# Kernel tuning notes

Hardware: AMD Instinct MI355X
Metric: run time of the kernel (lower is better)

## Reference

```python
import jax, jax.numpy as jnp
import numpy as np

EPS = 1e-5
SLOPE = 0.2

def _inorm(x):
    # InstanceNorm2d with affine=False on [B, C, N, 1]: normalize over spatial N per (b, c).
    mu = jnp.mean(x, axis=-1, keepdims=True)
    var = jnp.var(x, axis=-1, keepdims=True)  # biased variance, matches torch InstanceNorm
    return (x - mu) * jax.lax.rsqrt(var + EPS)

def _lrelu(x):
    return jnp.where(x >= 0, x, SLOPE * x)

def _block(W, x):
    # 1x1 conv (channel matmul) -> instance norm -> leaky relu; x: [B, Cin, N]
    return _lrelu(_inorm(jnp.einsum('oc,bcn->bon', W, x)))

def setup_inputs() -> dict:
    key = jax.random.key(0)
    k1, k2, k3, k4, k5 = jax.random.split(key, 5)
    B, C, N = 8, 256, 2048
    feat = jax.random.normal(k1, (B, C, N), dtype=jnp.float32)
    W1 = jax.random.normal(k2, (2 * C, C), dtype=jnp.float32) * (1.0 / np.sqrt(C))
    W2 = jax.random.normal(k3, (2 * C, C), dtype=jnp.float32) * (1.0 / np.sqrt(C))
    W3 = jax.random.normal(k4, (2 * C, C), dtype=jnp.float32) * (1.0 / np.sqrt(C))
    W4 = jax.random.normal(k5, (C, 2 * C), dtype=jnp.float32) * (1.0 / np.sqrt(2 * C))
    return {"feat": feat, "W1": W1, "W2": W2, "W3": W3, "W4": W4}

def reference(feat, W1, W2, W3, W4):
    # feat: [B, C, N]
    x1 = _block(W1, feat)  # [B, 2C, N]
    x2 = _block(W2, feat)  # [B, 2C, N]
    x3 = _block(W3, feat)  # [B, 2C, N]
    # query_key: x1^T @ x2 -> [B, N, N]
    qk = jnp.einsum('bcn,bcm->bnm', x1, x2)
    # x3 @ qk -> [B, 2C, N]; offset attention: subtract from x1
    x4 = x1 - jnp.einsum('bcn,bnm->bcm', x3, qk)
    out = _block(W4, x4)  # [B, C, N]
    return out
```

## Files before the change

kernel.cpp:

```cpp
#include <hip/hip_runtime.h>
#include <stdint.h>


#define LRELU_SLOPE 0.2f
#define EPS_IN 1e-5f

typedef __attribute__((ext_vector_type(8))) short short8v;
typedef __attribute__((ext_vector_type(4))) float f32x4;

__device__ __forceinline__ unsigned short f2bf(float f) {
    unsigned int u = __builtin_bit_cast(unsigned int, f);
    u = (u + 0x7fffu + ((u >> 16) & 1u)) >> 16;
    return (unsigned short)u;
}
__device__ __forceinline__ float bf2f(unsigned short h) {
    return __builtin_bit_cast(float, (unsigned int)h << 16);
}

typedef const __attribute__((address_space(1))) unsigned int* as1_uint_ptr;
typedef __attribute__((address_space(3))) unsigned int* as3_uint_ptr;

#define GLL16(g, l) __builtin_amdgcn_global_load_lds( \
    (as1_uint_ptr)(const void*)(g), (as3_uint_ptr)(void*)(l), 16, 0, 0)

enum { EP_F32 = 0, EP_BF16 = 1, EP_SUB_T_SPLIT = 2 };

template<int BM, int BN, int EP>
__global__ __launch_bounds__(256)
void gemm_tn(const unsigned short* __restrict__ A, const unsigned short* __restrict__ B,
             const unsigned short* __restrict__ Dm, void* __restrict__ Cv,
             int K, int lda, int ldb, int ldd, int ldc,
             int64_t sA, int64_t sB, int64_t sD, int64_t sC)
{
    constexpr int FM = BM / 32, FN = BN / 32;
    const int bz = blockIdx.z;
    A += sA * bz;
    B += sB * bz;

    const int i0 = blockIdx.y * BM;
    const int j0 = blockIdx.x * BN;

    __shared__ __align__(16) unsigned short As[BM * 32];
    __shared__ __align__(16) unsigned short Bs[BN * 32];

    const int t = threadIdx.x;
    const int w = t >> 6, l = t & 63;
    const int wr = w >> 1, wc = w & 1;

    f32x4 acc[FM][FN];
#pragma unroll
    for (int fm = 0; fm < FM; ++fm)
#pragma unroll
        for (int fn = 0; fn < FN; ++fn)
            acc[fm][fn] = (f32x4){0.f, 0.f, 0.f, 0.f};

    for (int k0 = 0; k0 < K; k0 += 32) {
        __syncthreads();
#pragma unroll
        for (int q = 0; q < BM / 64; ++q) {
            const int seg = w * (BM / 64) + q;
            const int row = seg * 16 + (l >> 2);
            const unsigned short* g = A + (size_t)(i0 + row) * lda + k0 + (l & 3) * 8;
            GLL16(g, &As[seg * 512]);
        }
#pragma unroll
        for (int q = 0; q < BN / 64; ++q) {
            const int seg = w * (BN / 64) + q;
            const int row = seg * 16 + (l >> 2);
            const unsigned short* g = B + (size_t)(j0 + row) * ldb + k0 + (l & 3) * 8;
            GLL16(g, &Bs[seg * 512]);
        }
        asm volatile("s_waitcnt vmcnt(0)" ::: "memory");
        __syncthreads();

        short8v a[FM], b[FN];
#pragma unroll
        for (int fm = 0; fm < FM; ++fm)
            a[fm] = *(const short8v*)&As[(wr * (BM / 2) + fm * 16 + (l & 15)) * 32 + (l >> 4) * 8];
#pragma unroll
        for (int fn = 0; fn < FN; ++fn)
            b[fn] = *(const short8v*)&Bs[(wc * (BN / 2) + fn * 16 + (l & 15)) * 32 + (l >> 4) * 8];
#pragma unroll
        for (int fm = 0; fm < FM; ++fm)
#pragma unroll
            for (int fn = 0; fn < FN; ++fn)
                acc[fm][fn] = __builtin_amdgcn_mfma_f32_16x16x32_bf16(a[fm], b[fn], acc[fm][fn], 0, 0, 0);
    }

    const int cr4 = (l >> 4) * 4;
    const int cc = l & 15;
#pragma unroll
    for (int fm = 0; fm < FM; ++fm) {
#pragma unroll
        for (int fn = 0; fn < FN; ++fn) {
            const int grow0 = i0 + wr * (BM / 2) + fm * 16 + cr4;
            const int gcol  = j0 + wc * (BN / 2) + fn * 16 + cc;
            if constexpr (EP == EP_F32) {
                float* C = (float*)Cv + sC * bz;
#pragma unroll
                for (int r = 0; r < 4; ++r)
                    C[(size_t)(grow0 + r) * ldc + gcol] = acc[fm][fn][r];
            } else if constexpr (EP == EP_BF16) {
                unsigned short* C = (unsigned short*)Cv + sC * bz;
#pragma unroll
                for (int r = 0; r < 4; ++r)
                    C[(size_t)(grow0 + r) * ldc + gcol] = f2bf(acc[fm][fn][r]);
            } else {
                const unsigned short* D = Dm + sD * bz;
                unsigned short* C = (unsigned short*)Cv + sC * bz;
                ushort4 hi4, lo4;
#pragma unroll
                for (int r = 0; r < 4; ++r) {
                    const float s = bf2f(D[(size_t)(grow0 + r) * ldd + gcol]) - acc[fm][fn][r];
                    const unsigned short h = f2bf(s);
                    const unsigned short lo = f2bf(s - bf2f(h));
                    ((unsigned short*)&hi4)[r] = h;
                    ((unsigned short*)&lo4)[r] = lo;
                }
                *(ushort4*)&C[(size_t)gcol * ldc + grow0] = hi4;
                *(ushort4*)&C[(size_t)gcol * ldc + (ldc >> 1) + grow0] = lo4;
            }
        }
    }
}

__global__ __launch_bounds__(256)
void row_norm_lrelu_bf16(unsigned short* __restrict__ y)
{
    const size_t row = blockIdx.x;
    uint4* p = (uint4*)(y + row * 2048);
    const int t = threadIdx.x;
    uint4 v = p[t];

    unsigned int wd[4] = {v.x, v.y, v.z, v.w};
    float f[8];
#pragma unroll
    for (int i = 0; i < 4; ++i) {
        f[2 * i]     = __builtin_bit_cast(float, wd[i] << 16);
        f[2 * i + 1] = __builtin_bit_cast(float, wd[i] & 0xffff0000u);
    }
    float s = 0.f, ss = 0.f;
#pragma unroll
    for (int i = 0; i < 8; ++i) { s += f[i]; ss += f[i] * f[i]; }

#pragma unroll
    for (int off = 32; off > 0; off >>= 1) {
        s  += __shfl_down(s, off, 64);
        ss += __shfl_down(ss, off, 64);
    }
    __shared__ float red[10];
    const int wid = t >> 6;
    if ((t & 63) == 0) { red[wid] = s; red[4 + wid] = ss; }
    __syncthreads();
    if (t == 0) {
        const float S  = red[0] + red[1] + red[2] + red[3];
        const float SS = red[4] + red[5] + red[6] + red[7];
        const float mu = S * (1.0f / 2048.0f);
        const float var = SS * (1.0f / 2048.0f) - mu * mu;
        red[8] = mu;
        red[9] = rsqrtf(var + EPS_IN);
    }
    __syncthreads();
    const float mu = red[8], rs = red[9];
#pragma unroll
    for (int i = 0; i < 8; ++i) {
        float e = (f[i] - mu) * rs;
        f[i] = (e >= 0.f) ? e : LRELU_SLOPE * e;
    }
#pragma unroll
    for (int i = 0; i < 4; ++i)
        wd[i] = (unsigned int)f2bf(f[2 * i]) | ((unsigned int)f2bf(f[2 * i + 1]) << 16);
    p[t] = make_uint4(wd[0], wd[1], wd[2], wd[3]);
}

__global__ __launch_bounds__(256)
void row_norm_lrelu(const float* __restrict__ in, float* __restrict__ out)
{
    const size_t row = blockIdx.x;
    const float4* p = (const float4*)(in + row * 2048);
    float4* q = (float4*)(out + row * 2048);
    const int t = threadIdx.x;

    float4 v0 = p[t];
    float4 v1 = p[t + 256];

    float s  = v0.x + v0.y + v0.z + v0.w + v1.x + v1.y + v1.z + v1.w;
    float ss = v0.x * v0.x + v0.y * v0.y + v0.z * v0.z + v0.w * v0.w +
               v1.x * v1.x + v1.y * v1.y + v1.z * v1.z + v1.w * v1.w;
#pragma unroll
    for (int off = 32; off > 0; off >>= 1) {
        s  += __shfl_down(s, off, 64);
        ss += __shfl_down(ss, off, 64);
    }
    __shared__ float red[10];
    const int wid = t >> 6;
    if ((t & 63) == 0) { red[wid] = s; red[4 + wid] = ss; }
    __syncthreads();
    if (t == 0) {
        const float S  = red[0] + red[1] + red[2] + red[3];
        const float SS = red[4] + red[5] + red[6] + red[7];
        const float mu = S * (1.0f / 2048.0f);
        const float var = SS * (1.0f / 2048.0f) - mu * mu;
        red[8] = mu;
        red[9] = rsqrtf(var + EPS_IN);
    }
    __syncthreads();
    const float mu = red[8], rs = red[9];
#define NRM(x) { float e = ((x) - mu) * rs; (x) = (e >= 0.0f) ? e : LRELU_SLOPE * e; }
    NRM(v0.x) NRM(v0.y) NRM(v0.z) NRM(v0.w)
    NRM(v1.x) NRM(v1.y) NRM(v1.z) NRM(v1.w)
#undef NRM
    q[t] = v0;
    q[t + 256] = v1;
}

template<bool F32IN>
__global__ __launch_bounds__(256)
void transpose_cast(const void* __restrict__ in, unsigned short* __restrict__ out,
                    int inCols, int outCols, int64_t sIn, int64_t sOut)
{
    __shared__ __align__(16) unsigned short tile[64][68];
    const int t = threadIdx.x;
    const int r0 = blockIdx.y * 64, c0 = blockIdx.x * 64;
    const int ir = t >> 4, ic = (t & 15) * 4;

#pragma unroll
    for (int q = 0; q < 4; ++q) {
        const int rr = q * 16 + ir;
        if constexpr (F32IN) {
            const float* ip = (const float*)in + sIn * blockIdx.z + (size_t)(r0 + rr) * inCols + c0 + ic;
            float4 v = *(const float4*)ip;
            tile[rr][ic + 0] = f2bf(v.x);
            tile[rr][ic + 1] = f2bf(v.y);
            tile[rr][ic + 2] = f2bf(v.z);
            tile[rr][ic + 3] = f2bf(v.w);
        } else {
            const unsigned short* ip = (const unsigned short*)in + sIn * blockIdx.z + (size_t)(r0 + rr) * inCols + c0 + ic;
            ushort4 v = *(const ushort4*)ip;
            tile[rr][ic + 0] = v.x;
            tile[rr][ic + 1] = v.y;
            tile[rr][ic + 2] = v.z;
            tile[rr][ic + 3] = v.w;
        }
    }
    __syncthreads();

    const int n = t & 63, kc = (t >> 6) * 16;
    unsigned short* op = out + sOut * blockIdx.z + (size_t)(c0 + n) * outCols + r0 + kc;
    unsigned int wo[8];
#pragma unroll
    for (int i = 0; i < 8; ++i)
        wo[i] = (unsigned int)tile[kc + 2 * i][n] | ((unsigned int)tile[kc + 2 * i + 1][n] << 16);
    *(uint4*)op       = make_uint4(wo[0], wo[1], wo[2], wo[3]);
    *(uint4*)(op + 8) = make_uint4(wo[4], wo[5], wo[6], wo[7]);
}

__global__ __launch_bounds__(256)
void cast_weights(const float* __restrict__ W1, const float* __restrict__ W2,
                  const float* __restrict__ W3, const float* __restrict__ W4,
                  unsigned short* __restrict__ Wcatb, unsigned short* __restrict__ W4cat)
{
    const int wsel = blockIdx.x >> 7;
    const int local = ((blockIdx.x & 127) * 256 + threadIdx.x) * 4;
    const float* src = (wsel == 0) ? W1 : (wsel == 1) ? W2 : (wsel == 2) ? W3 : W4;
    float4 v = *(const float4*)(src + local);
    ushort4 pk = make_ushort4(f2bf(v.x), f2bf(v.y), f2bf(v.z), f2bf(v.w));
    if (wsel < 3) {
        *(ushort4*)(Wcatb + (size_t)wsel * 131072 + local) = pk;
    } else {
        const int o = local >> 9, c = local & 511;
        *(ushort4*)(W4cat + (size_t)o * 1024 + c)       = pk;
        *(ushort4*)(W4cat + (size_t)o * 1024 + 512 + c) = pk;
    }
}

extern "C" void kernel_launch(void* const* d_in, const int* in_sizes, int n_in,
                              void* d_out, int out_size, void* d_ws, size_t ws_size,
                              hipStream_t stream)
{
    const float* feat = (const float*)d_in[0];
    const float* W1   = (const float*)d_in[1];
    const float* W2   = (const float*)d_in[2];
    const float* W3   = (const float*)d_in[3];
    const float* W4   = (const float*)d_in[4];
    float* out = (float*)d_out;

    char* w = (char*)d_ws;
    unsigned short* ybf   = (unsigned short*)(w + 0);
    unsigned short* featT = (unsigned short*)(w + 50331648);
    unsigned short* x2T   = (unsigned short*)(w + 58720256);
    unsigned short* Amb   = (unsigned short*)(w + 75497472);
    unsigned short* x4Ts  = (unsigned short*)(w + 79691776);
    float*          z     = (float*)(w + 113246208);
    unsigned short* Wcatb = (unsigned short*)(w + 130023424);
    unsigned short* W4cat = (unsigned short*)(w + 130809856);

    cast_weights<<<512, 256, 0, stream>>>(W1, W2, W3, W4, Wcatb, W4cat);

    transpose_cast<true><<<dim3(32, 4, 8), 256, 0, stream>>>(
        feat, featT, 2048, 256, 524288, 524288);

    gemm_tn<128, 128, EP_BF16><<<dim3(16, 12, 8), 256, 0, stream>>>(
        Wcatb, featT, nullptr, ybf,
        256, 256, 256, 0, 2048,
        0, 524288, 0, 3145728);

    row_norm_lrelu_bf16<<<12288, 256, 0, stream>>>(ybf);

    transpose_cast<false><<<dim3(32, 8, 8), 256, 0, stream>>>(
        ybf + 1048576, x2T, 2048, 512, 3145728, 1048576);

    gemm_tn<64, 64, EP_BF16><<<dim3(8, 8, 8), 256, 0, stream>>>(
        ybf + 2097152, ybf, nullptr, Amb,
        2048, 2048, 2048, 0, 512,
        3145728, 3145728, 0, 262144);

    gemm_tn<128, 128, EP_SUB_T_SPLIT><<<dim3(16, 4, 8), 256, 0, stream>>>(
        Amb, x2T, ybf, x4Ts,
        512, 512, 512, 2048, 1024,
        262144, 1048576, 3145728, 2097152);

    gemm_tn<128, 128, EP_F32><<<dim3(16, 2, 8), 256, 0, stream>>>(
        W4cat, x4Ts, nullptr, z,
        1024, 1024, 1024, 0, 2048,
        0, 2097152, 0, 524288);

    row_norm_lrelu<<<2048, 256, 0, stream>>>(z, out);
}
```

Measured before the change: 221.8 us.

## Fuse instance-norm statistics into GEMM epilogues and apply normalization on load

The first projection GEMM now emits per-row partial sums and sums of squares, and a small kernel reduces them to mean and rstd. The norm+lrelu is applied lazily where the data is consumed: when loading operands for the x3·x1 GEMM, in the x2 transpose, and in the subtract epilogue. This removes the separate read-modify-write normalization pass over the large activation buffer. The final GEMM becomes a cooperative kernel that computes row stats, does a grid-wide sync and writes the normalized output directly, dropping the fp32 intermediate and its norm kernel. In exchange the attention GEMM loses its async global-to-LDS loads in favour of register loads plus normalization, and the cooperative launch needs all 256 blocks resident at once.

```diff
diff --git a/kernel.cpp b/kernel.cpp
--- a/kernel.cpp
+++ b/kernel.cpp
@@ -1,4 +1,5 @@
 #include <hip/hip_runtime.h>
+#include <hip/hip_cooperative_groups.h>
 #include <stdint.h>
 
 
@@ -23,12 +24,13 @@
 #define GLL16(g, l) __builtin_amdgcn_global_load_lds( \
     (as1_uint_ptr)(const void*)(g), (as3_uint_ptr)(void*)(l), 16, 0, 0)
 
-enum { EP_F32 = 0, EP_BF16 = 1, EP_SUB_T_SPLIT = 2 };
+enum { EP_BF16_STATS = 0, EP_SUB_T_SPLIT_NORM = 1 };
 
 template<int BM, int BN, int EP>
 __global__ __launch_bounds__(256)
 void gemm_tn(const unsigned short* __restrict__ A, const unsigned short* __restrict__ B,
              const unsigned short* __restrict__ Dm, void* __restrict__ Cv,
+             const float2* __restrict__ stats, float2* __restrict__ part,
              int K, int lda, int ldb, int ldd, int ldc,
              int64_t sA, int64_t sB, int64_t sD, int64_t sC)
 {
@@ -60,15 +62,13 @@
         for (int q = 0; q < BM / 64; ++q) {
             const int seg = w * (BM / 64) + q;
             const int row = seg * 16 + (l >> 2);
-            const unsigned short* g = A + (size_t)(i0 + row) * lda + k0 + (l & 3) * 8;
-            GLL16(g, &As[seg * 512]);
+            GLL16(A + (size_t)(i0 + row) * lda + k0 + (l & 3) * 8, &As[seg * 512]);
         }
 #pragma unroll
         for (int q = 0; q < BN / 64; ++q) {
             const int seg = w * (BN / 64) + q;
             const int row = seg * 16 + (l >> 2);
-            const unsigned short* g = B + (size_t)(j0 + row) * ldb + k0 + (l & 3) * 8;
-            GLL16(g, &Bs[seg * 512]);
+            GLL16(B + (size_t)(j0 + row) * ldb + k0 + (l & 3) * 8, &Bs[seg * 512]);
         }
         asm volatile("s_waitcnt vmcnt(0)" ::: "memory");
         __syncthreads();
@@ -89,33 +89,58 @@
 
     const int cr4 = (l >> 4) * 4;
     const int cc = l & 15;
-#pragma unroll
-    for (int fm = 0; fm < FM; ++fm) {
-#pragma unroll
-        for (int fn = 0; fn < FN; ++fn) {
+
+    if constexpr (EP == EP_BF16_STATS) {
+        unsigned short* C = (unsigned short*)Cv + sC * bz;
+        __shared__ float2 wp[2][BM];
+#pragma unroll
+        for (int fm = 0; fm < FM; ++fm) {
+#pragma unroll
+            for (int r = 0; r < 4; ++r) {
+                float s = 0.f, q = 0.f;
+#pragma unroll
+                for (int fn = 0; fn < FN; ++fn) {
+                    const float v = acc[fm][fn][r];
+                    s += v; q += v * v;
+                    C[(size_t)(i0 + wr * (BM / 2) + fm * 16 + cr4 + r) * ldc +
+                      (j0 + wc * (BN / 2) + fn * 16 + cc)] = f2bf(v);
+                }
+#pragma unroll
+                for (int m = 1; m < 16; m <<= 1) {
+                    s += __shfl_xor(s, m, 64);
+                    q += __shfl_xor(q, m, 64);
+                }
+                if ((l & 15) == 0)
+                    wp[wc][wr * (BM / 2) + fm * 16 + cr4 + r] = make_float2(s, q);
+            }
+        }
+        __syncthreads();
+        if (t < BM) {
+            const float2 p0 = wp[0][t], p1 = wp[1][t];
+            part[(size_t)(bz * 1536 + i0 + t) * gridDim.x + blockIdx.x] =
+                make_float2(p0.x + p1.x, p0.y + p1.y);
+        }
+    } else {
+        const unsigned short* D = Dm + sD * bz;
+        unsigned short* C = (unsigned short*)Cv + sC * bz;
+#pragma unroll
+        for (int fm = 0; fm < FM; ++fm) {
             const int grow0 = i0 + wr * (BM / 2) + fm * 16 + cr4;
-            const int gcol  = j0 + wc * (BN / 2) + fn * 16 + cc;
-            if constexpr (EP == EP_F32) {
-                float* C = (float*)Cv + sC * bz;
-#pragma unroll
-                for (int r = 0; r < 4; ++r)
-                    C[(size_t)(grow0 + r) * ldc + gcol] = acc[fm][fn][r];
-            } else if constexpr (EP == EP_BF16) {
-                unsigned short* C = (unsigned short*)Cv + sC * bz;
-#pragma unroll
-                for (int r = 0; r < 4; ++r)
-                    C[(size_t)(grow0 + r) * ldc + gcol] = f2bf(acc[fm][fn][r]);
-            } else {
-                const unsigned short* D = Dm + sD * bz;
-                unsigned short* C = (unsigned short*)Cv + sC * bz;
+            float2 st[4];
+#pragma unroll
+            for (int r = 0; r < 4; ++r) st[r] = stats[bz * 1536 + grow0 + r];
+#pragma unroll
+            for (int fn = 0; fn < FN; ++fn) {
+                const int gcol = j0 + wc * (BN / 2) + fn * 16 + cc;
                 ushort4 hi4, lo4;
 #pragma unroll
                 for (int r = 0; r < 4; ++r) {
-                    const float s = bf2f(D[(size_t)(grow0 + r) * ldd + gcol]) - acc[fm][fn][r];
-                    const unsigned short h = f2bf(s);
-                    const unsigned short lo = f2bf(s - bf2f(h));
+                    float dv = (bf2f(D[(size_t)(grow0 + r) * ldd + gcol]) - st[r].x) * st[r].y;
+                    dv = dv >= 0.f ? dv : LRELU_SLOPE * dv;
+                    const float sv = dv - acc[fm][fn][r];
+                    const unsigned short h = f2bf(sv);
                     ((unsigned short*)&hi4)[r] = h;
-                    ((unsigned short*)&lo4)[r] = lo;
+                    ((unsigned short*)&lo4)[r] = f2bf(sv - bf2f(h));
                 }
                 *(ushort4*)&C[(size_t)gcol * ldc + grow0] = hi4;
                 *(ushort4*)&C[(size_t)gcol * ldc + (ldc >> 1) + grow0] = lo4;
@@ -125,128 +150,244 @@
 }
 
 __global__ __launch_bounds__(256)
-void row_norm_lrelu_bf16(unsigned short* __restrict__ y)
-{
-    const size_t row = blockIdx.x;
-    uint4* p = (uint4*)(y + row * 2048);
-    const int t = threadIdx.x;
-    uint4 v = p[t];
-
-    unsigned int wd[4] = {v.x, v.y, v.z, v.w};
-    float f[8];
+void reduce_stats(const float2* __restrict__ part, float2* __restrict__ stats)
+{
+    const int row = blockIdx.x * 256 + threadIdx.x;
+    float S = 0.f, Q = 0.f;
+#pragma unroll
+    for (int j = 0; j < 16; ++j) {
+        const float2 p = part[(size_t)row * 16 + j];
+        S += p.x; Q += p.y;
+    }
+    const float mu = S * (1.0f / 2048.0f);
+    const float var = Q * (1.0f / 2048.0f) - mu * mu;
+    stats[row] = make_float2(mu, rsqrtf(var + EPS_IN));
+}
+
+__device__ __forceinline__ void norm_store8(unsigned short* dst, uint4 v, float2 st)
+{
+    const unsigned int wd[4] = {v.x, v.y, v.z, v.w};
+    unsigned int o[4];
 #pragma unroll
     for (int i = 0; i < 4; ++i) {
-        f[2 * i]     = __builtin_bit_cast(float, wd[i] << 16);
-        f[2 * i + 1] = __builtin_bit_cast(float, wd[i] & 0xffff0000u);
-    }
-    float s = 0.f, ss = 0.f;
-#pragma unroll
-    for (int i = 0; i < 8; ++i) { s += f[i]; ss += f[i] * f[i]; }
-
-#pragma unroll
-    for (int off = 32; off > 0; off >>= 1) {
-        s  += __shfl_down(s, off, 64);
-        ss += __shfl_down(ss, off, 64);
-    }
-    __shared__ float red[10];
-    const int wid = t >> 6;
-    if ((t & 63) == 0) { red[wid] = s; red[4 + wid] = ss; }
+        float a = __builtin_bit_cast(float, wd[i] << 16);
+        float b = __builtin_bit_cast(float, wd[i] & 0xffff0000u);
+        a = (a - st.x) * st.y; a = a >= 0.f ? a : LRELU_SLOPE * a;
+        b = (b - st.x) * st.y; b = b >= 0.f ? b : LRELU_SLOPE * b;
+        o[i] = (unsigned int)f2bf(a) | ((unsigned int)f2bf(b) << 16);
+    }
+    *(uint4*)dst = make_uint4(o[0], o[1], o[2], o[3]);
+}
+
+__global__ __launch_bounds__(256)
+void gemm_am(const unsigned short* __restrict__ ybf, const float2* __restrict__ stats,
+             unsigned short* __restrict__ Amb)
+{
+    const int bz = blockIdx.z;
+    const unsigned short* Yb = ybf + (size_t)bz * 3145728;
+    const int i0 = blockIdx.y * 128;
+    const int j0 = blockIdx.x * 64;
+
+    __shared__ __align__(16) unsigned short As[128 * 32];
+    __shared__ __align__(16) unsigned short Bs[64 * 32];
+
+    const int t = threadIdx.x, w = t >> 6, l = t & 63;
+    const int wr = w >> 1, wc = w & 1;
+    const int lr = l >> 2, lk = (l & 3) * 8;
+
+    const int rA0 = i0 + (w * 2 + 0) * 16 + lr;
+    const int rA1 = i0 + (w * 2 + 1) * 16 + lr;
+    const int rB  = j0 + w * 16 + lr;
+    const float2 stA0 = stats[bz * 1536 + 1024 + rA0];
+    const float2 stA1 = stats[bz * 1536 + 1024 + rA1];
+    const float2 stB  = stats[bz * 1536 + rB];
+    const unsigned short* gA0 = Yb + (size_t)(1024 + rA0) * 2048 + lk;
+    const unsigned short* gA1 = Yb + (size_t)(1024 + rA1) * 2048 + lk;
+    const unsigned short* gB  = Yb + (size_t)rB * 2048 + lk;
+
+    f32x4 acc[4][2];
+#pragma unroll
+    for (int fm = 0; fm < 4; ++fm)
+#pragma unroll
+        for (int fn = 0; fn < 2; ++fn)
+            acc[fm][fn] = (f32x4){0.f, 0.f, 0.f, 0.f};
+
+    for (int k0 = 0; k0 < 2048; k0 += 32) {
+        const uint4 vA0 = *(const uint4*)(gA0 + k0);
+        const uint4 vA1 = *(const uint4*)(gA1 + k0);
+        const uint4 vB  = *(const uint4*)(gB + k0);
+        __syncthreads();
+        norm_store8(&As[(w * 2 + 0) * 512 + l * 8], vA0, stA0);
+        norm_store8(&As[(w * 2 + 1) * 512 + l * 8], vA1, stA1);
+        norm_store8(&Bs[w * 512 + l * 8], vB, stB);
+        __syncthreads();
+
+        short8v a[4], b[2];
+#pragma unroll
+        for (int fm = 0; fm < 4; ++fm)
+            a[fm] = *(const short8v*)&As[(wr * 64 + fm * 16 + (l & 15)) * 32 + (l >> 4) * 8];
+#pragma unroll
+        for (int fn = 0; fn < 2; ++fn)
+            b[fn] = *(const short8v*)&Bs[(wc * 32 + fn * 16 + (l & 15)) * 32 + (l >> 4) * 8];
+#pragma unroll
+        for (int fm = 0; fm < 4; ++fm)
+#pragma unroll
+            for (int fn = 0; fn < 2; ++fn)
+                acc[fm][fn] = __builtin_amdgcn_mfma_f32_16x16x32_bf16(a[fm], b[fn], acc[fm][fn], 0, 0, 0);
+    }
+
+    unsigned short* C = Amb + (size_t)bz * 262144;
+    const int cr4 = (l >> 4) * 4, cc = l & 15;
+#pragma unroll
+    for (int fm = 0; fm < 4; ++fm)
+#pragma unroll
+        for (int fn = 0; fn < 2; ++fn)
+#pragma unroll
+            for (int r = 0; r < 4; ++r)
+                C[(size_t)(i0 + wr * 64 + fm * 16 + cr4 + r) * 512 +
+                  (j0 + wc * 32 + fn * 16 + cc)] = f2bf(acc[fm][fn][r]);
+}
+
+__global__ __launch_bounds__(256)
+void gemm_z_coop(const unsigned short* __restrict__ A, const unsigned short* __restrict__ Bg,
+                 float2* __restrict__ zpart, float* __restrict__ out)
+{
+    const int bz = blockIdx.z;
+    const unsigned short* B = Bg + (size_t)bz * 2097152;
+    const int i0 = blockIdx.y * 128;
+    const int j0 = blockIdx.x * 128;
+
+    __shared__ __align__(16) unsigned short As[128 * 32];
+    __shared__ __align__(16) unsigned short Bs[128 * 32];
+
+    const int t = threadIdx.x, w = t >> 6, l = t & 63;
+    const int wr = w >> 1, wc = w & 1;
+
+    f32x4 acc[4][4];
+#pragma unroll
+    for (int fm = 0; fm < 4; ++fm)
+#pragma unroll
+        for (int fn = 0; fn < 4; ++fn)
+            acc[fm][fn] = (f32x4){0.f, 0.f, 0.f, 0.f};
+
+    for (int k0 = 0; k0 < 1024; k0 += 32) {
+        __syncthreads();
+#pragma unroll
+        for (int q = 0; q < 2; ++q) {
+            const int seg = w * 2 + q;
+            const int row = seg * 16 + (l >> 2);
+            GLL16(A + (size_t)(i0 + row) * 1024 + k0 + (l & 3) * 8, &As[seg * 512]);
+            GLL16(B + (size_t)(j0 + row) * 1024 + k0 + (l & 3) * 8, &Bs[seg * 512]);
+        }
+        asm volatile("s_waitcnt vmcnt(0)" ::: "memory");
+        __syncthreads();
+
+        short8v a[4], b[4];
+#pragma unroll
+        for (int fm = 0; fm < 4; ++fm)
+            a[fm] = *(const short8v*)&As[(wr * 64 + fm * 16 + (l & 15)) * 32 + (l >> 4) * 8];
+#pragma unroll
+        for (int fn = 0; fn < 4; ++fn)
+            b[fn] = *(const short8v*)&Bs[(wc * 64 + fn * 16 + (l & 15)) * 32 + (l >> 4) * 8];
+#pragma unroll
+        for (int fm = 0; fm < 4; ++fm)
+#pragma unroll
+            for (int fn = 0; fn < 4; ++fn)
+                acc[fm][fn] = __builtin_amdgcn_mfma_f32_16x16x32_bf16(a[fm], b[fn], acc[fm][fn], 0, 0, 0);
+    }
+
+    const int cr4 = (l >> 4) * 4, cc = l & 15;
+
+    __shared__ float2 wp[2][128];
+#pragma unroll
+    for (int fm = 0; fm < 4; ++fm) {
+#pragma unroll
+        for (int r = 0; r < 4; ++r) {
+            float s = 0.f, q = 0.f;
+#pragma unroll
+            for (int fn = 0; fn < 4; ++fn) {
+                const float v = acc[fm][fn][r];
+                s += v; q += v * v;
+            }
+#pragma unroll
+            for (int m = 1; m < 16; m <<= 1) {
+                s += __shfl_xor(s, m, 64);
+                q += __shfl_xor(q, m, 64);
+            }
+            if ((l & 15) == 0) wp[wc][wr * 64 + fm * 16 + cr4 + r] = make_float2(s, q);
+        }
+    }
     __syncthreads();
-    if (t == 0) {
-        const float S  = red[0] + red[1] + red[2] + red[3];
-        const float SS = red[4] + red[5] + red[6] + red[7];
+    if (t < 128) {
+        const float2 p0 = wp[0][t], p1 = wp[1][t];
+        zpart[((size_t)bz * 256 + i0 + t) * 16 + blockIdx.x] = make_float2(p0.x + p1.x, p0.y + p1.y);
+    }
+    __threadfence();
+    cooperative_groups::this_grid().sync();
+
+    __shared__ float2 rst[128];
+    if (t < 128) {
+        float S = 0.f, Q = 0.f;
+#pragma unroll
+        for (int j = 0; j < 16; ++j) {
+            const float2 p = zpart[((size_t)bz * 256 + i0 + t) * 16 + j];
+            S += p.x; Q += p.y;
+        }
         const float mu = S * (1.0f / 2048.0f);
-        const float var = SS * (1.0f / 2048.0f) - mu * mu;
-        red[8] = mu;
-        red[9] = rsqrtf(var + EPS_IN);
+        const float var = Q * (1.0f / 2048.0f) - mu * mu;
+        rst[t] = make_float2(mu, rsqrtf(var + EPS_IN));
     }
     __syncthreads();
-    const float mu = red[8], rs = red[9];
-#pragma unroll
-    for (int i = 0; i < 8; ++i) {
-        float e = (f[i] - mu) * rs;
-        f[i] = (e >= 0.f) ? e : LRELU_SLOPE * e;
-    }
-#pragma unroll
-    for (int i = 0; i < 4; ++i)
-        wd[i] = (unsigned int)f2bf(f[2 * i]) | ((unsigned int)f2bf(f[2 * i + 1]) << 16);
-    p[t] = make_uint4(wd[0], wd[1], wd[2], wd[3]);
-}
-
-__global__ __launch_bounds__(256)
-void row_norm_lrelu(const float* __restrict__ in, float* __restrict__ out)
-{
-    const size_t row = blockIdx.x;
-    const float4* p = (const float4*)(in + row * 2048);
-    float4* q = (float4*)(out + row * 2048);
-    const int t = threadIdx.x;
-
-    float4 v0 = p[t];
-    float4 v1 = p[t + 256];
-
-    float s  = v0.x + v0.y + v0.z + v0.w + v1.x + v1.y + v1.z + v1.w;
-    float ss = v0.x * v0.x + v0.y * v0.y + v0.z * v0.z + v0.w * v0.w +
-               v1.x * v1.x + v1.y * v1.y + v1.z * v1.z + v1.w * v1.w;
-#pragma unroll
-    for (int off = 32; off > 0; off >>= 1) {
-        s  += __shfl_down(s, off, 64);
-        ss += __shfl_down(ss, off, 64);
-    }
-    __shared__ float red[10];
-    const int wid = t >> 6;
-    if ((t & 63) == 0) { red[wid] = s; red[4 + wid] = ss; }
-    __syncthreads();
-    if (t == 0) {
-        const float S  = red[0] + red[1] + red[2] + red[3];
-        const float SS = red[4] + red[5] + red[6] + red[7];
-        const float mu = S * (1.0f / 2048.0f);
-        const float var = SS * (1.0f / 2048.0f) - mu * mu;
-        red[8] = mu;
-        red[9] = rsqrtf(var + EPS_IN);
-    }
-    __syncthreads();
-    const float mu = red[8], rs = red[9];
-#define NRM(x) { float e = ((x) - mu) * rs; (x) = (e >= 0.0f) ? e : LRELU_SLOPE * e; }
-    NRM(v0.x) NRM(v0.y) NRM(v0.z) NRM(v0.w)
-    NRM(v1.x) NRM(v1.y) NRM(v1.z) NRM(v1.w)
-#undef NRM
-    q[t] = v0;
-    q[t + 256] = v1;
-}
-
-template<bool F32IN>
-__global__ __launch_bounds__(256)
-void transpose_cast(const void* __restrict__ in, unsigned short* __restrict__ out,
-                    int inCols, int outCols, int64_t sIn, int64_t sOut)
+
+    float* O = out + (size_t)bz * 524288;
+#pragma unroll
+    for (int fm = 0; fm < 4; ++fm) {
+        const int lrow0 = wr * 64 + fm * 16 + cr4;
+        float2 st[4];
+#pragma unroll
+        for (int r = 0; r < 4; ++r) st[r] = rst[lrow0 + r];
+#pragma unroll
+        for (int fn = 0; fn < 4; ++fn) {
+            const int gcol = j0 + wc * 64 + fn * 16 + cc;
+#pragma unroll
+            for (int r = 0; r < 4; ++r) {
+                float e = (acc[fm][fn][r] - st[r].x) * st[r].y;
+                e = e >= 0.f ? e : LRELU_SLOPE * e;
+                O[(size_t)(i0 + lrow0 + r) * 2048 + gcol] = e;
+            }
+        }
+    }
+}
+
+__global__ __launch_bounds__(256)
+void transpose_norm_x2(const unsigned short* __restrict__ ybf,
+                       const float2* __restrict__ stats,
+                       unsigned short* __restrict__ x2T)
 {
     __shared__ __align__(16) unsigned short tile[64][68];
-    const int t = threadIdx.x;
+    const int t = threadIdx.x, bz = blockIdx.z;
+    const unsigned short* in = ybf + (size_t)bz * 3145728 + (size_t)512 * 2048;
+    unsigned short* outp = x2T + (size_t)bz * 1048576;
     const int r0 = blockIdx.y * 64, c0 = blockIdx.x * 64;
     const int ir = t >> 4, ic = (t & 15) * 4;
 
 #pragma unroll
     for (int q = 0; q < 4; ++q) {
         const int rr = q * 16 + ir;
-        if constexpr (F32IN) {
-            const float* ip = (const float*)in + sIn * blockIdx.z + (size_t)(r0 + rr) * inCols + c0 + ic;
-            float4 v = *(const float4*)ip;
-            tile[rr][ic + 0] = f2bf(v.x);
-            tile[rr][ic + 1] = f2bf(v.y);
-            tile[rr][ic + 2] = f2bf(v.z);
-            tile[rr][ic + 3] = f2bf(v.w);
-        } else {
-            const unsigned short* ip = (const unsigned short*)in + sIn * blockIdx.z + (size_t)(r0 + rr) * inCols + c0 + ic;
-            ushort4 v = *(const ushort4*)ip;
-            tile[rr][ic + 0] = v.x;
-            tile[rr][ic + 1] = v.y;
-            tile[rr][ic + 2] = v.z;
-            tile[rr][ic + 3] = v.w;
+        const float2 st = stats[bz * 1536 + 512 + r0 + rr];
+        const ushort4 v = *(const ushort4*)&in[(size_t)(r0 + rr) * 2048 + c0 + ic];
+        const unsigned short vv[4] = {v.x, v.y, v.z, v.w};
+#pragma unroll
+        for (int j = 0; j < 4; ++j) {
+            float e = (bf2f(vv[j]) - st.x) * st.y;
+            e = e >= 0.f ? e : LRELU_SLOPE * e;
+            tile[rr][ic + j] = f2bf(e);
         }
     }
     __syncthreads();
 
     const int n = t & 63, kc = (t >> 6) * 16;
-    unsigned short* op = out + sOut * blockIdx.z + (size_t)(c0 + n) * outCols + r0 + kc;
+    unsigned short* op = outp + (size_t)(c0 + n) * 512 + r0 + kc;
     unsigned int wo[8];
 #pragma unroll
     for (int i = 0; i < 8; ++i)
@@ -256,6 +397,37 @@
 }
 
 __global__ __launch_bounds__(256)
+void transpose_feat(const float* __restrict__ in, unsigned short* __restrict__ out)
+{
+    __shared__ __align__(16) unsigned short tile[64][68];
+    const int t = threadIdx.x, bz = blockIdx.z;
+    const float* ip0 = in + (size_t)bz * 524288;
+    unsigned short* outp = out + (size_t)bz * 524288;
+    const int r0 = blockIdx.y * 64, c0 = blockIdx.x * 64;
+    const int ir = t >> 4, ic = (t & 15) * 4;
+
+#pragma unroll
+    for (int q = 0; q < 4; ++q) {
+        const int rr = q * 16 + ir;
+        const float4 v = *(const float4*)&ip0[(size_t)(r0 + rr) * 2048 + c0 + ic];
+        tile[rr][ic + 0] = f2bf(v.x);
+        tile[rr][ic + 1] = f2bf(v.y);
+        tile[rr][ic + 2] = f2bf(v.z);
+        tile[rr][ic + 3] = f2bf(v.w);
+    }
+    __syncthreads();
+
+    const int n = t & 63, kc = (t >> 6) * 16;
+    unsigned short* op = outp + (size_t)(c0 + n) * 256 + r0 + kc;
+    unsigned int wo[8];
+#pragma unroll
+    for (int i = 0; i < 8; ++i)
+        wo[i] = (unsigned int)tile[kc + 2 * i][n] | ((unsigned int)tile[kc + 2 * i + 1][n] << 16);
+    *(uint4*)op       = make_uint4(wo[0], wo[1], wo[2], wo[3]);
+    *(uint4*)(op + 8) = make_uint4(wo[4], wo[5], wo[6], wo[7]);
+}
+
+__global__ __launch_bounds__(256)
 void cast_weights(const float* __restrict__ W1, const float* __restrict__ W2,
                   const float* __restrict__ W3, const float* __restrict__ W4,
                   unsigned short* __restrict__ Wcatb, unsigned short* __restrict__ W4cat)
@@ -263,8 +435,8 @@
     const int wsel = blockIdx.x >> 7;
     const int local = ((blockIdx.x & 127) * 256 + threadIdx.x) * 4;
     const float* src = (wsel == 0) ? W1 : (wsel == 1) ? W2 : (wsel == 2) ? W3 : W4;
-    float4 v = *(const float4*)(src + local);
-    ushort4 pk = make_ushort4(f2bf(v.x), f2bf(v.y), f2bf(v.z), f2bf(v.w));
+    const float4 v = *(const float4*)(src + local);
+    const ushort4 pk = make_ushort4(f2bf(v.x), f2bf(v.y), f2bf(v.z), f2bf(v.w));
     if (wsel < 3) {
         *(ushort4*)(Wcatb + (size_t)wsel * 131072 + local) = pk;
     } else {
@@ -291,39 +463,37 @@
     unsigned short* x2T   = (unsigned short*)(w + 58720256);
     unsigned short* Amb   = (unsigned short*)(w + 75497472);
     unsigned short* x4Ts  = (unsigned short*)(w + 79691776);
-    float*          z     = (float*)(w + 113246208);
-    unsigned short* Wcatb = (unsigned short*)(w + 130023424);
-    unsigned short* W4cat = (unsigned short*)(w + 130809856);
+    unsigned short* Wcatb = (unsigned short*)(w + 113246208);
+    unsigned short* W4cat = (unsigned short*)(w + 114032640);
+    float2*         part1 = (float2*)(w + 114556928);
+    float2*         stats = (float2*)(w + 116129792);
+    float2*         zpart = (float2*)(w + 116228096);
 
     cast_weights<<<512, 256, 0, stream>>>(W1, W2, W3, W4, Wcatb, W4cat);
 
-    transpose_cast<true><<<dim3(32, 4, 8), 256, 0, stream>>>(
-        feat, featT, 2048, 256, 524288, 524288);
-
-    gemm_tn<128, 128, EP_BF16><<<dim3(16, 12, 8), 256, 0, stream>>>(
-        Wcatb, featT, nullptr, ybf,
-        256, 256, 256, 0, 2048,
-        0, 524288, 0, 3145728);
-
-    row_norm_lrelu_bf16<<<12288, 256, 0, stream>>>(ybf);
-
-    transpose_cast<false><<<dim3(32, 8, 8), 256, 0, stream>>>(
-        ybf + 1048576, x2T, 2048, 512, 3145728, 1048576);
-
-    gemm_tn<64, 64, EP_BF16><<<dim3(8, 8, 8), 256, 0, stream>>>(
-        ybf + 2097152, ybf, nullptr, Amb,
-        2048, 2048, 2048, 0, 512,
-        3145728, 3145728, 0, 262144);
-
-    gemm_tn<128, 128, EP_SUB_T_SPLIT><<<dim3(16, 4, 8), 256, 0, stream>>>(
-        Amb, x2T, ybf, x4Ts,
-        512, 512, 512, 2048, 1024,
-        262144, 1048576, 3145728, 2097152);
-
-    gemm_tn<128, 128, EP_F32><<<dim3(16, 2, 8), 256, 0, stream>>>(
-        W4cat, x4Ts, nullptr, z,
-        1024, 1024, 1024, 0, 2048,
-        0, 2097152, 0, 524288);
-
-    row_norm_lrelu<<<2048, 256, 0, stream>>>(z, out);
-}
+    transpose_feat<<<dim3(32, 4, 8), 256, 0, stream>>>(feat, featT);
+
+    gemm_tn<128, 128, EP_BF16_STATS><<<dim3(16, 12, 8), 256, 0, stream>>>(
+        Wcatb, featT, nullptr, ybf, nullptr, part1,
+        256, 256, 256, 0, 2048, 0, 524288, 0, 3145728);
+
+    reduce_stats<<<48, 256, 0, stream>>>(part1, stats);
+
+    transpose_norm_x2<<<dim3(32, 8, 8), 256, 0, stream>>>(ybf, stats, x2T);
+
+    gemm_am<<<dim3(8, 4, 8), 256, 0, stream>>>(ybf, stats, Amb);
+
+    gemm_tn<128, 128, EP_SUB_T_SPLIT_NORM><<<dim3(16, 4, 8), 256, 0, stream>>>(
+        Amb, x2T, ybf, x4Ts, stats, nullptr,
+        512, 512, 512, 2048, 1024, 262144, 1048576, 3145728, 2097152);
+
+    {
+        const unsigned short* a0 = W4cat;
+        const unsigned short* b0 = x4Ts;
+        float2* zp = zpart;
+        float* o0 = out;
+        void* zargs[4] = {&a0, &b0, &zp, &o0};
+        hipLaunchCooperativeKernel((const void*)gemm_z_coop, dim3(16, 2, 8),
+                                   dim3(256, 1, 1), zargs, 0, stream);
+    }
+}
```

After: 346.3 us. +56.1%, slower.

## Fuse instance-norm statistics into first GEMM epilogue and normalize during transpose

Applied to the files above, without the earlier changes.

The first projection GEMM now computes per-row partial sums and sums of squares in its epilogue, and a small kernel reduces them into mean and rstd. This replaces the separate in-place row-norm pass over the 12288 rows. Normalization and leaky ReLU are applied while transposing x2 and while copying x1/x3 into a compact buffer, so the statistics are no longer recomputed from bf16 reads. The last GEMM's tile changes to 128x64 for more blocks, and the workspace layout is repacked. The cost is an extra reduction launch, a norm copy kernel, and statistics taken from fp32 accumulators rather than bf16-rounded values.

```diff
diff --git a/kernel.cpp b/kernel.cpp
--- a/kernel.cpp
+++ b/kernel.cpp
@@ -23,12 +23,13 @@
 #define GLL16(g, l) __builtin_amdgcn_global_load_lds( \
     (as1_uint_ptr)(const void*)(g), (as3_uint_ptr)(void*)(l), 16, 0, 0)
 
-enum { EP_F32 = 0, EP_BF16 = 1, EP_SUB_T_SPLIT = 2 };
+enum { EP_F32 = 0, EP_BF16 = 1, EP_SUB_T_SPLIT = 2, EP_BF16_STATS = 3 };
 
 template<int BM, int BN, int EP>
 __global__ __launch_bounds__(256)
 void gemm_tn(const unsigned short* __restrict__ A, const unsigned short* __restrict__ B,
              const unsigned short* __restrict__ Dm, void* __restrict__ Cv,
+             float2* __restrict__ part,
              int K, int lda, int ldb, int ldd, int ldc,
              int64_t sA, int64_t sB, int64_t sD, int64_t sC)
 {
@@ -60,15 +61,13 @@
         for (int q = 0; q < BM / 64; ++q) {
             const int seg = w * (BM / 64) + q;
             const int row = seg * 16 + (l >> 2);
-            const unsigned short* g = A + (size_t)(i0 + row) * lda + k0 + (l & 3) * 8;
-            GLL16(g, &As[seg * 512]);
+            GLL16(A + (size_t)(i0 + row) * lda + k0 + (l & 3) * 8, &As[seg * 512]);
         }
 #pragma unroll
         for (int q = 0; q < BN / 64; ++q) {
             const int seg = w * (BN / 64) + q;
             const int row = seg * 16 + (l >> 2);
-            const unsigned short* g = B + (size_t)(j0 + row) * ldb + k0 + (l & 3) * 8;
-            GLL16(g, &Bs[seg * 512]);
+            GLL16(B + (size_t)(j0 + row) * ldb + k0 + (l & 3) * 8, &Bs[seg * 512]);
         }
         asm volatile("s_waitcnt vmcnt(0)" ::: "memory");
         __syncthreads();
@@ -89,60 +88,205 @@
 
     const int cr4 = (l >> 4) * 4;
     const int cc = l & 15;
-#pragma unroll
-    for (int fm = 0; fm < FM; ++fm) {
-#pragma unroll
-        for (int fn = 0; fn < FN; ++fn) {
+
+    if constexpr (EP == EP_F32) {
+        float* C = (float*)Cv + sC * bz;
+#pragma unroll
+        for (int fm = 0; fm < FM; ++fm)
+#pragma unroll
+            for (int fn = 0; fn < FN; ++fn)
+#pragma unroll
+                for (int r = 0; r < 4; ++r)
+                    C[(size_t)(i0 + wr * (BM / 2) + fm * 16 + cr4 + r) * ldc +
+                      (j0 + wc * (BN / 2) + fn * 16 + cc)] = acc[fm][fn][r];
+    } else if constexpr (EP == EP_BF16) {
+        unsigned short* C = (unsigned short*)Cv + sC * bz;
+#pragma unroll
+        for (int fm = 0; fm < FM; ++fm)
+#pragma unroll
+            for (int fn = 0; fn < FN; ++fn)
+#pragma unroll
+                for (int r = 0; r < 4; ++r)
+                    C[(size_t)(i0 + wr * (BM / 2) + fm * 16 + cr4 + r) * ldc +
+                      (j0 + wc * (BN / 2) + fn * 16 + cc)] = f2bf(acc[fm][fn][r]);
+    } else if constexpr (EP == EP_SUB_T_SPLIT) {
+        const unsigned short* D = Dm + sD * bz;
+        unsigned short* C = (unsigned short*)Cv + sC * bz;
+#pragma unroll
+        for (int fm = 0; fm < FM; ++fm) {
             const int grow0 = i0 + wr * (BM / 2) + fm * 16 + cr4;
-            const int gcol  = j0 + wc * (BN / 2) + fn * 16 + cc;
-            if constexpr (EP == EP_F32) {
-                float* C = (float*)Cv + sC * bz;
-#pragma unroll
-                for (int r = 0; r < 4; ++r)
-                    C[(size_t)(grow0 + r) * ldc + gcol] = acc[fm][fn][r];
-            } else if constexpr (EP == EP_BF16) {
-                unsigned short* C = (unsigned short*)Cv + sC * bz;
-#pragma unroll
-                for (int r = 0; r < 4; ++r)
-                    C[(size_t)(grow0 + r) * ldc + gcol] = f2bf(acc[fm][fn][r]);
-            } else {
-                const unsigned short* D = Dm + sD * bz;
-                unsigned short* C = (unsigned short*)Cv + sC * bz;
+#pragma unroll
+            for (int fn = 0; fn < FN; ++fn) {
+                const int gcol = j0 + wc * (BN / 2) + fn * 16 + cc;
                 ushort4 hi4, lo4;
 #pragma unroll
                 for (int r = 0; r < 4; ++r) {
-                    const float s = bf2f(D[(size_t)(grow0 + r) * ldd + gcol]) - acc[fm][fn][r];
-                    const unsigned short h = f2bf(s);
-                    const unsigned short lo = f2bf(s - bf2f(h));
+                    const float sv = bf2f(D[(size_t)(grow0 + r) * ldd + gcol]) - acc[fm][fn][r];
+                    const unsigned short h = f2bf(sv);
                     ((unsigned short*)&hi4)[r] = h;
-                    ((unsigned short*)&lo4)[r] = lo;
+                    ((unsigned short*)&lo4)[r] = f2bf(sv - bf2f(h));
                 }
                 *(ushort4*)&C[(size_t)gcol * ldc + grow0] = hi4;
                 *(ushort4*)&C[(size_t)gcol * ldc + (ldc >> 1) + grow0] = lo4;
             }
         }
-    }
-}
-
-__global__ __launch_bounds__(256)
-void row_norm_lrelu_bf16(unsigned short* __restrict__ y)
+    } else {
+        unsigned short* C = (unsigned short*)Cv + sC * bz;
+        __shared__ float2 wp[2][BM];
+#pragma unroll
+        for (int fm = 0; fm < FM; ++fm) {
+#pragma unroll
+            for (int r = 0; r < 4; ++r) {
+                float s = 0.f, q = 0.f;
+#pragma unroll
+                for (int fn = 0; fn < FN; ++fn) {
+                    const float v = acc[fm][fn][r];
+                    s += v; q += v * v;
+                    C[(size_t)(i0 + wr * (BM / 2) + fm * 16 + cr4 + r) * ldc +
+                      (j0 + wc * (BN / 2) + fn * 16 + cc)] = f2bf(v);
+                }
+#pragma unroll
+                for (int m = 1; m < 16; m <<= 1) {
+                    s += __shfl_xor(s, m, 64);
+                    q += __shfl_xor(q, m, 64);
+                }
+                if ((l & 15) == 0)
+                    wp[wc][wr * (BM / 2) + fm * 16 + cr4 + r] = make_float2(s, q);
+            }
+        }
+        __syncthreads();
+        if (t < BM) {
+            const float2 p0 = wp[0][t], p1 = wp[1][t];
+            part[(size_t)(bz * 1536 + i0 + t) * gridDim.x + blockIdx.x] =
+                make_float2(p0.x + p1.x, p0.y + p1.y);
+        }
+    }
+}
+
+__global__ __launch_bounds__(256)
+void reduce_stats(const float2* __restrict__ part, float2* __restrict__ stats)
+{
+    const int row = blockIdx.x * 256 + threadIdx.x;
+    float S = 0.f, Q = 0.f;
+#pragma unroll
+    for (int j = 0; j < 16; ++j) {
+        const float2 p = part[(size_t)row * 16 + j];
+        S += p.x; Q += p.y;
+    }
+    const float mu = S * (1.0f / 2048.0f);
+    const float var = Q * (1.0f / 2048.0f) - mu * mu;
+    stats[row] = make_float2(mu, rsqrtf(var + EPS_IN));
+}
+
+__device__ __forceinline__ uint4 norm8(uint4 v, float2 st)
+{
+    const unsigned int wd[4] = {v.x, v.y, v.z, v.w};
+    unsigned int o[4];
+#pragma unroll
+    for (int i = 0; i < 4; ++i) {
+        float a = __builtin_bit_cast(float, wd[i] << 16);
+        float b = __builtin_bit_cast(float, wd[i] & 0xffff0000u);
+        a = (a - st.x) * st.y; a = a >= 0.f ? a : LRELU_SLOPE * a;
+        b = (b - st.x) * st.y; b = b >= 0.f ? b : LRELU_SLOPE * b;
+        o[i] = (unsigned int)f2bf(a) | ((unsigned int)f2bf(b) << 16);
+    }
+    return make_uint4(o[0], o[1], o[2], o[3]);
+}
+
+__global__ __launch_bounds__(256)
+void norm12(const unsigned short* __restrict__ ybf, const float2* __restrict__ stats,
+            unsigned short* __restrict__ x1n3)
+{
+    const int bz = blockIdx.y;
+    const int x = blockIdx.x;
+    const int src = (x < 512) ? x : (x + 512);
+    const float2 st = stats[bz * 1536 + src];
+    const uint4 v = ((const uint4*)(ybf + (size_t)bz * 3145728 + (size_t)src * 2048))[threadIdx.x];
+    ((uint4*)(x1n3 + (size_t)bz * 2097152 + (size_t)x * 2048))[threadIdx.x] = norm8(v, st);
+}
+
+__global__ __launch_bounds__(256)
+void transpose_norm_x2(const unsigned short* __restrict__ ybf,
+                       const float2* __restrict__ stats,
+                       unsigned short* __restrict__ x2T)
+{
+    __shared__ __align__(16) unsigned short tile[64][68];
+    const int t = threadIdx.x, bz = blockIdx.z;
+    const unsigned short* in = ybf + (size_t)bz * 3145728 + (size_t)512 * 2048;
+    unsigned short* outp = x2T + (size_t)bz * 1048576;
+    const int r0 = blockIdx.y * 64, c0 = blockIdx.x * 64;
+    const int ir = t >> 4, ic = (t & 15) * 4;
+
+#pragma unroll
+    for (int q = 0; q < 4; ++q) {
+        const int rr = q * 16 + ir;
+        const float2 st = stats[bz * 1536 + 512 + r0 + rr];
+        const ushort4 v = *(const ushort4*)&in[(size_t)(r0 + rr) * 2048 + c0 + ic];
+        const unsigned short vv[4] = {v.x, v.y, v.z, v.w};
+#pragma unroll
+        for (int j = 0; j < 4; ++j) {
+            float e = (bf2f(vv[j]) - st.x) * st.y;
+            e = e >= 0.f ? e : LRELU_SLOPE * e;
+            tile[rr][ic + j] = f2bf(e);
+        }
+    }
+    __syncthreads();
+
+    const int n = t & 63, kc = (t >> 6) * 16;
+    unsigned short* op = outp + (size_t)(c0 + n) * 512 + r0 + kc;
+    unsigned int wo[8];
+#pragma unroll
+    for (int i = 0; i < 8; ++i)
+        wo[i] = (unsigned int)tile[kc + 2 * i][n] | ((unsigned int)tile[kc + 2 * i + 1][n] << 16);
+    *(uint4*)op       = make_uint4(wo[0], wo[1], wo[2], wo[3]);
+    *(uint4*)(op + 8) = make_uint4(wo[4], wo[5], wo[6], wo[7]);
+}
+
+__global__ __launch_bounds__(256)
+void transpose_feat(const float* __restrict__ in, unsigned short* __restrict__ out)
+{
+    __shared__ __align__(16) unsigned short tile[64][68];
+    const int t = threadIdx.x, bz = blockIdx.z;
+    const float* ip0 = in + (size_t)bz * 524288;
+    unsigned short* outp = out + (size_t)bz * 524288;
+    const int r0 = blockIdx.y * 64, c0 = blockIdx.x * 64;
+    const int ir = t >> 4, ic = (t & 15) * 4;
+
+#pragma unroll
+    for (int q = 0; q < 4; ++q) {
+        const int rr = q * 16 + ir;
+        const float4 v = *(const float4*)&ip0[(size_t)(r0 + rr) * 2048 + c0 + ic];
+        tile[rr][ic + 0] = f2bf(v.x);
+        tile[rr][ic + 1] = f2bf(v.y);
+        tile[rr][ic + 2] = f2bf(v.z);
+        tile[rr][ic + 3] = f2bf(v.w);
+    }
+    __syncthreads();
+
+    const int n = t & 63, kc = (t >> 6) * 16;
+    unsigned short* op = outp + (size_t)(c0 + n) * 256 + r0 + kc;
+    unsigned int wo[8];
+#pragma unroll
+    for (int i = 0; i < 8; ++i)
+        wo[i] = (unsigned int)tile[kc + 2 * i][n] | ((unsigned int)tile[kc + 2 * i + 1][n] << 16);
+    *(uint4*)op       = make_uint4(wo[0], wo[1], wo[2], wo[3]);
+    *(uint4*)(op + 8) = make_uint4(wo[4], wo[5], wo[6], wo[7]);
+}
+
+__global__ __launch_bounds__(256)
+void row_norm_lrelu(const float* __restrict__ in, float* __restrict__ out)
 {
     const size_t row = blockIdx.x;
-    uint4* p = (uint4*)(y + row * 2048);
+    const float4* p = (const float4*)(in + row * 2048);
+    float4* q = (float4*)(out + row * 2048);
     const int t = threadIdx.x;
-    uint4 v = p[t];
-
-    unsigned int wd[4] = {v.x, v.y, v.z, v.w};
-    float f[8];
-#pragma unroll
-    for (int i = 0; i < 4; ++i) {
-        f[2 * i]     = __builtin_bit_cast(float, wd[i] << 16);
-        f[2 * i + 1] = __builtin_bit_cast(float, wd[i] & 0xffff0000u);
-    }
-    float s = 0.f, ss = 0.f;
-#pragma unroll
-    for (int i = 0; i < 8; ++i) { s += f[i]; ss += f[i] * f[i]; }
-
+
+    float4 v0 = p[t];
+    float4 v1 = p[t + 256];
+
+    float s  = v0.x + v0.y + v0.z + v0.w + v1.x + v1.y + v1.z + v1.w;
+    float ss = v0.x * v0.x + v0.y * v0.y + v0.z * v0.z + v0.w * v0.w +
+               v1.x * v1.x + v1.y * v1.y + v1.z * v1.z + v1.w * v1.w;
 #pragma unroll
     for (int off = 32; off > 0; off >>= 1) {
         s  += __shfl_down(s, off, 64);
@@ -162,50 +306,6 @@
     }
     __syncthreads();
     const float mu = red[8], rs = red[9];
-#pragma unroll
-    for (int i = 0; i < 8; ++i) {
-        float e = (f[i] - mu) * rs;
-        f[i] = (e >= 0.f) ? e : LRELU_SLOPE * e;
-    }
-#pragma unroll
-    for (int i = 0; i < 4; ++i)
-        wd[i] = (unsigned int)f2bf(f[2 * i]) | ((unsigned int)f2bf(f[2 * i + 1]) << 16);
-    p[t] = make_uint4(wd[0], wd[1], wd[2], wd[3]);
-}
-
-__global__ __launch_bounds__(256)
-void row_norm_lrelu(const float* __restrict__ in, float* __restrict__ out)
-{
-    const size_t row = blockIdx.x;
-    const float4* p = (const float4*)(in + row * 2048);
-    float4* q = (float4*)(out + row * 2048);
-    const int t = threadIdx.x;
-
-    float4 v0 = p[t];
-    float4 v1 = p[t + 256];
-
-    float s  = v0.x + v0.y + v0.z + v0.w + v1.x + v1.y + v1.z + v1.w;
-    float ss = v0.x * v0.x + v0.y * v0.y + v0.z * v0.z + v0.w * v0.w +
-               v1.x * v1.x + v1.y * v1.y + v1.z * v1.z + v1.w * v1.w;
-#pragma unroll
-    for (int off = 32; off > 0; off >>= 1) {
-        s  += __shfl_down(s, off, 64);
-        ss += __shfl_down(ss, off, 64);
-    }
-    __shared__ float red[10];
-    const int wid = t >> 6;
-    if ((t & 63) == 0) { red[wid] = s; red[4 + wid] = ss; }
-    __syncthreads();
-    if (t == 0) {
-        const float S  = red[0] + red[1] + red[2] + red[3];
-        const float SS = red[4] + red[5] + red[6] + red[7];
-        const float mu = S * (1.0f / 2048.0f);
-        const float var = SS * (1.0f / 2048.0f) - mu * mu;
-        red[8] = mu;
-        red[9] = rsqrtf(var + EPS_IN);
-    }
-    __syncthreads();
-    const float mu = red[8], rs = red[9];
 #define NRM(x) { float e = ((x) - mu) * rs; (x) = (e >= 0.0f) ? e : LRELU_SLOPE * e; }
     NRM(v0.x) NRM(v0.y) NRM(v0.z) NRM(v0.w)
     NRM(v1.x) NRM(v1.y) NRM(v1.z) NRM(v1.w)
@@ -214,47 +314,6 @@
     q[t + 256] = v1;
 }
 
-template<bool F32IN>
-__global__ __launch_bounds__(256)
-void transpose_cast(const void* __restrict__ in, unsigned short* __restrict__ out,
-                    int inCols, int outCols, int64_t sIn, int64_t sOut)
-{
-    __shared__ __align__(16) unsigned short tile[64][68];
-    const int t = threadIdx.x;
-    const int r0 = blockIdx.y * 64, c0 = blockIdx.x * 64;
-    const int ir = t >> 4, ic = (t & 15) * 4;
-
-#pragma unroll
-    for (int q = 0; q < 4; ++q) {
-        const int rr = q * 16 + ir;
-        if constexpr (F32IN) {
-            const float* ip = (const float*)in + sIn * blockIdx.z + (size_t)(r0 + rr) * inCols + c0 + ic;
-            float4 v = *(const float4*)ip;
-            tile[rr][ic + 0] = f2bf(v.x);
-            tile[rr][ic + 1] = f2bf(v.y);
-            tile[rr][ic + 2] = f2bf(v.z);
-            tile[rr][ic + 3] = f2bf(v.w);
-        } else {
-            const unsigned short* ip = (const unsigned short*)in + sIn * blockIdx.z + (size_t)(r0 + rr) * inCols + c0 + ic;
-            ushort4 v = *(const ushort4*)ip;
-            tile[rr][ic + 0] = v.x;
-            tile[rr][ic + 1] = v.y;
-            tile[rr][ic + 2] = v.z;
-            tile[rr][ic + 3] = v.w;
-        }
-    }
-    __syncthreads();
-
-    const int n = t & 63, kc = (t >> 6) * 16;
-    unsigned short* op = out + sOut * blockIdx.z + (size_t)(c0 + n) * outCols + r0 + kc;
-    unsigned int wo[8];
-#pragma unroll
-    for (int i = 0; i < 8; ++i)
-        wo[i] = (unsigned int)tile[kc + 2 * i][n] | ((unsigned int)tile[kc + 2 * i + 1][n] << 16);
-    *(uint4*)op       = make_uint4(wo[0], wo[1], wo[2], wo[3]);
-    *(uint4*)(op + 8) = make_uint4(wo[4], wo[5], wo[6], wo[7]);
-}
-
 __global__ __launch_bounds__(256)
 void cast_weights(const float* __restrict__ W1, const float* __restrict__ W2,
                   const float* __restrict__ W3, const float* __restrict__ W4,
@@ -263,8 +322,8 @@
     const int wsel = blockIdx.x >> 7;
     const int local = ((blockIdx.x & 127) * 256 + threadIdx.x) * 4;
     const float* src = (wsel == 0) ? W1 : (wsel == 1) ? W2 : (wsel == 2) ? W3 : W4;
-    float4 v = *(const float4*)(src + local);
-    ushort4 pk = make_ushort4(f2bf(v.x), f2bf(v.y), f2bf(v.z), f2bf(v.w));
+    const float4 v = *(const float4*)(src + local);
+    const ushort4 pk = make_ushort4(f2bf(v.x), f2bf(v.y), f2bf(v.z), f2bf(v.w));
     if (wsel < 3) {
         *(ushort4*)(Wcatb + (size_t)wsel * 131072 + local) = pk;
     } else {
@@ -287,43 +346,41 @@
 
     char* w = (char*)d_ws;
     unsigned short* ybf   = (unsigned short*)(w + 0);
+    unsigned short* x4Ts  = (unsigned short*)(w + 0);
+    float*          z     = (float*)(w + 33554432);
     unsigned short* featT = (unsigned short*)(w + 50331648);
     unsigned short* x2T   = (unsigned short*)(w + 58720256);
-    unsigned short* Amb   = (unsigned short*)(w + 75497472);
-    unsigned short* x4Ts  = (unsigned short*)(w + 79691776);
-    float*          z     = (float*)(w + 113246208);
-    unsigned short* Wcatb = (unsigned short*)(w + 130023424);
-    unsigned short* W4cat = (unsigned short*)(w + 130809856);
+    unsigned short* x1n3  = (unsigned short*)(w + 75497472);
+    unsigned short* Amb   = (unsigned short*)(w + 109051904);
+    unsigned short* Wcatb = (unsigned short*)(w + 113246208);
+    unsigned short* W4cat = (unsigned short*)(w + 114032640);
+    float2*         part1 = (float2*)(w + 114556928);
+    float2*         stats = (float2*)(w + 116129792);
 
     cast_weights<<<512, 256, 0, stream>>>(W1, W2, W3, W4, Wcatb, W4cat);
 
-    transpose_cast<true><<<dim3(32, 4, 8), 256, 0, stream>>>(
-        feat, featT, 2048, 256, 524288, 524288);
-
-    gemm_tn<128, 128, EP_BF16><<<dim3(16, 12, 8), 256, 0, stream>>>(
-        Wcatb, featT, nullptr, ybf,
-        256, 256, 256, 0, 2048,
-        0, 524288, 0, 3145728);
-
-    row_norm_lrelu_bf16<<<12288, 256, 0, stream>>>(ybf);
-
-    transpose_cast<false><<<dim3(32, 8, 8), 256, 0, stream>>>(
-        ybf + 1048576, x2T, 2048, 512, 3145728, 1048576);
+    transpose_feat<<<dim3(32, 4, 8), 256, 0, stream>>>(feat, featT);
+
+    gemm_tn<128, 128, EP_BF16_STATS><<<dim3(16, 12, 8), 256, 0, stream>>>(
+        Wcatb, featT, nullptr, ybf, part1,
+        256, 256, 256, 0, 2048, 0, 524288, 0, 3145728);
+
+    reduce_stats<<<48, 256, 0, stream>>>(part1, stats);
+
+    transpose_norm_x2<<<dim3(32, 8, 8), 256, 0, stream>>>(ybf, stats, x2T);
+    norm12<<<dim3(1024, 8), 256, 0, stream>>>(ybf, stats, x1n3);
 
     gemm_tn<64, 64, EP_BF16><<<dim3(8, 8, 8), 256, 0, stream>>>(
-        ybf + 2097152, ybf, nullptr, Amb,
-        2048, 2048, 2048, 0, 512,
-        3145728, 3145728, 0, 262144);
+        x1n3 + 1048576 , x1n3 , nullptr, Amb, nullptr,
+        2048, 2048, 2048, 0, 512, 2097152, 2097152, 0, 262144);
 
     gemm_tn<128, 128, EP_SUB_T_SPLIT><<<dim3(16, 4, 8), 256, 0, stream>>>(
-        Amb, x2T, ybf, x4Ts,
-        512, 512, 512, 2048, 1024,
-        262144, 1048576, 3145728, 2097152);
-
-    gemm_tn<128, 128, EP_F32><<<dim3(16, 2, 8), 256, 0, stream>>>(
-        W4cat, x4Ts, nullptr, z,
-        1024, 1024, 1024, 0, 2048,
-        0, 2097152, 0, 524288);
+        Amb, x2T, x1n3, x4Ts, nullptr,
+        512, 512, 512, 2048, 1024, 262144, 1048576, 2097152, 2097152);
+
+    gemm_tn<128, 64, EP_F32><<<dim3(32, 2, 8), 256, 0, stream>>>(
+        W4cat, x4Ts, nullptr, z, nullptr,
+        1024, 1024, 1024, 0, 2048, 0, 2097152, 0, 524288);
 
     row_norm_lrelu<<<2048, 256, 0, stream>>>(z, out);
 }
```

After: 224.2 us. No clear change (+1.1%).
